# Optimization experiments

Measured on AMD Instinct MI355X. Metric: run time of the kernel, lower is better.

The kernel has to match this reference:

```python
import jax, jax.numpy as jnp
import numpy as np

E = 2_000_000   # edges
N = 200_000     # atoms
B = 100         # bond types (10 species, ordered pairs)
R = 13          # reduced_matrix_element (SK integrals per bond)
G = 512         # num_xgrid
T = 10          # atom types
OE = 4          # n_onsite_Es
R_MIN, R_MAX = 1.0, 6.0  # SK table distance range (Bohr-ish)


def setup_inputs() -> dict:
    key = jax.random.key(0)
    k1, k2, k3, k4, k5, k6 = jax.random.split(key, 6)
    rij = jax.random.uniform(k1, (E,), jnp.float32, 1.5, 5.5)
    edge_type = jax.random.randint(k2, (E,), 0, B, jnp.int32)
    atom_type = jax.random.randint(k3, (N,), 0, T, jnp.int32)
    xx = jnp.linspace(R_MIN, R_MAX, G, dtype=jnp.float32)  # sorted distance grid
    hopping_param = jax.random.normal(k4, (B, R, G), jnp.float32)
    overlap_param = jax.random.normal(k5, (B, R, G), jnp.float32)
    onsite_param = jax.random.normal(k6, (T, OE, 1), jnp.float32)
    return {"rij": rij, "edge_type": edge_type, "atom_type": atom_type,
            "xx": xx, "hopping_param": hopping_param,
            "overlap_param": overlap_param, "onsite_param": onsite_param}


def _interp_by_type(rij, edge_type, xx, table):
    """Fused gather + linear interpolation, keyed by edge_type.

    Replaces the original per-bond-type masked loop: for each edge, pick the
    [R, G] SK table for its bond type and linearly interpolate along the
    distance grid at rij. Returns [E, R].
    """
    g = xx.shape[0]
    # interval index for each edge (clamped -> linear extrapolation at edges)
    idx = jnp.clip(jnp.searchsorted(xx, rij, side="right") - 1, 0, g - 2)  # [E]
    x0 = xx[idx]
    x1 = xx[idx + 1]
    t = ((rij - x0) / (x1 - x0))[:, None]  # [E, 1]
    # advanced indexing on axes 0 and 2, full slice on axis 1 -> [E, R]
    y0 = table[edge_type, :, idx]
    y1 = table[edge_type, :, idx + 1]
    return y0 * (1.0 - t) + y1 * t


def reference(rij, edge_type, atom_type, xx, hopping_param, overlap_param, onsite_param):
    edge_features = _interp_by_type(rij, edge_type, xx, hopping_param)   # [E, R]
    edge_overlap = _interp_by_type(rij, edge_type, xx, overlap_param)    # [E, R]
    # dftb onsite: direct per-atom-type parameter lookup (num_paras == 1)
    node_features = onsite_param[atom_type, :, 0]                         # [N, OE]
    return edge_features, edge_overlap, node_features
```

## Files before the change

kernel.cpp:

```cpp
#include <hip/hip_runtime.h>

#define E_CNT 2000000
#define N_CNT 200000
#define B_CNT 100
#define R_CNT 13
#define G_CNT 512
#define T_CNT 10
#define OE_CNT 4

#define P_STRIDE 32
#define P_FLOATS ((size_t)B_CNT * G_CNT * P_STRIDE)
#define P_BYTES  (P_FLOATS * 4)

#define EDGES_PER_BLOCK 64
#define EDGE_BLOCKS (E_CNT / EDGES_PER_BLOCK)
#define NODE_BLOCKS ((N_CNT + 255) / 256)
#define OUT_OVL_OFF ((size_t)E_CNT * R_CNT)
#define OUT_NODE_OFF ((size_t)2 * E_CNT * R_CNT)

__global__ __launch_bounds__(256) void repack_kernel(
    const float* __restrict__ hopping,
    const float* __restrict__ overlap,
    float* __restrict__ P)
{
    int tid = blockIdx.x * 256 + threadIdx.x;
    const int total = B_CNT * R_CNT * G_CNT;
    if (tid >= total) return;
    int g = tid & (G_CNT - 1);
    int br = tid >> 9;
    int r = br % R_CNT;
    int b = br / R_CNT;
    size_t src = (size_t)tid;
    size_t dst = ((size_t)(b * G_CNT + g)) * P_STRIDE + r;
    P[dst] = hopping[src];
    P[dst + 16] = overlap[src];
}

__global__ __launch_bounds__(256) void dftbsk_main(
    const float* __restrict__ rij,
    const float* __restrict__ edge_type,
    const int* __restrict__ edge_type_i,
    const int* __restrict__ atom_type,
    const float* __restrict__ xx,
    const float* __restrict__ P,
    const float* __restrict__ onsite,
    float* __restrict__ out)
{
    if (blockIdx.x < EDGE_BLOCKS) {
        __shared__ float sxx[G_CNT];
        __shared__ float sh[EDGES_PER_BLOCK * 26];

        for (int i = threadIdx.x; i < G_CNT; i += 256) sxx[i] = xx[i];
        __syncthreads();

        int tid = threadIdx.x;
        int eL = tid >> 2;
        int j  = tid & 3;
        int e  = blockIdx.x * EDGES_PER_BLOCK + eL;

        float r = rij[e];
        int b = edge_type_i[e];

        const float inv_dx = (float)(G_CNT - 1) / 5.0f;
        int idx = (int)floorf((r - 1.0f) * inv_dx);
        idx = max(0, min(G_CNT - 2, idx));
        while (idx > 0 && r < sxx[idx]) --idx;
        while (idx < G_CNT - 2 && r >= sxx[idx + 1]) ++idx;

        float x0 = sxx[idx];
        float x1 = sxx[idx + 1];
        float t = (r - x0) / (x1 - x0);
        float omt = 1.0f - t;

        size_t base = ((size_t)(b * G_CNT + idx)) * P_STRIDE + 4 * j;
        float4 h0 = *(const float4*)(P + base);
        float4 h1 = *(const float4*)(P + base + P_STRIDE);
        float4 o0 = *(const float4*)(P + base + 16);
        float4 o1 = *(const float4*)(P + base + 16 + P_STRIDE);

        float4 v, w;
        v.x = h0.x * omt + h1.x * t;  v.y = h0.y * omt + h1.y * t;
        v.z = h0.z * omt + h1.z * t;  v.w = h0.w * omt + h1.w * t;
        w.x = o0.x * omt + o1.x * t;  w.y = o0.y * omt + o1.y * t;
        w.z = o0.z * omt + o1.z * t;  w.w = o0.w * omt + o1.w * t;

        int r0 = 4 * j;
        float* row = sh + eL * 26;
        {
            const float vv[4] = {v.x, v.y, v.z, v.w};
            const float ww[4] = {w.x, w.y, w.z, w.w};
            #pragma unroll
            for (int k = 0; k < 4; ++k) {
                int rr = r0 + k;
                if (rr < R_CNT) {
                    row[rr] = vv[k];
                    row[13 + rr] = ww[k];
                }
            }
        }
        __syncthreads();

        size_t hopBase = (size_t)blockIdx.x * (EDGES_PER_BLOCK * R_CNT);
        #pragma unroll
        for (int L = 0; L < 2; ++L) {
            int idx4 = tid + L * 256;
            if (idx4 < 416) {
                bool isOvl = idx4 >= 208;
                unsigned f0 = (unsigned)(isOvl ? (idx4 - 208) : idx4) * 4u;
                float4 q;
                float* qs = (float*)&q;
                #pragma unroll
                for (int k = 0; k < 4; ++k) {
                    unsigned f = f0 + k;
                    unsigned ee = f / 13u;
                    unsigned rr = f - ee * 13u;
                    qs[k] = sh[ee * 26 + (isOvl ? 13 : 0) + rr];
                }
                float* dst = out + (isOvl ? OUT_OVL_OFF : 0) + hopBase + f0;
                *(float4*)dst = q;
            }
        }
    } else {
        int n = (blockIdx.x - EDGE_BLOCKS) * 256 + threadIdx.x;
        if (n < N_CNT) {
            int t = atom_type[n];
            float4 v;
            v.x = onsite[t * OE_CNT + 0];
            v.y = onsite[t * OE_CNT + 1];
            v.z = onsite[t * OE_CNT + 2];
            v.w = onsite[t * OE_CNT + 3];
            *(float4*)(out + OUT_NODE_OFF + (size_t)n * OE_CNT) = v;
        }
    }
}

__global__ __launch_bounds__(256) void dftbsk_fallback(
    const float* __restrict__ rij,
    const int*   __restrict__ edge_type,
    const int*   __restrict__ atom_type,
    const float* __restrict__ xx,
    const float* __restrict__ hopping,
    const float* __restrict__ overlap,
    const float* __restrict__ onsite,
    float*       __restrict__ out)
{
    __shared__ float sxx[G_CNT];
    for (int i = threadIdx.x; i < G_CNT; i += blockDim.x) sxx[i] = xx[i];
    __syncthreads();

    long long gid = (long long)blockIdx.x * blockDim.x + threadIdx.x;
    if (gid < E_CNT) {
        int e = (int)gid;
        float r = rij[e];
        int b = edge_type[e];
        const float inv_dx = (float)(G_CNT - 1) / 5.0f;
        int idx = (int)floorf((r - 1.0f) * inv_dx);
        idx = max(0, min(G_CNT - 2, idx));
        while (idx > 0 && r < sxx[idx]) --idx;
        while (idx < G_CNT - 2 && r >= sxx[idx + 1]) ++idx;
        float x0 = sxx[idx], x1 = sxx[idx + 1];
        float t = (r - x0) / (x1 - x0);
        float omt = 1.0f - t;
        const float* hb = hopping + (size_t)b * (R_CNT * G_CNT) + idx;
        const float* ob = overlap + (size_t)b * (R_CNT * G_CNT) + idx;
        float* outh = out + (size_t)e * R_CNT;
        float* outo = out + OUT_OVL_OFF + (size_t)e * R_CNT;
        #pragma unroll
        for (int rr = 0; rr < R_CNT; ++rr)
            outh[rr] = hb[rr * G_CNT] * omt + hb[rr * G_CNT + 1] * t;
        #pragma unroll
        for (int rr = 0; rr < R_CNT; ++rr)
            outo[rr] = ob[rr * G_CNT] * omt + ob[rr * G_CNT + 1] * t;
    } else if (gid < (long long)E_CNT + N_CNT) {
        int n = (int)(gid - E_CNT);
        int t = atom_type[n];
        float4 v;
        v.x = onsite[t * OE_CNT + 0];
        v.y = onsite[t * OE_CNT + 1];
        v.z = onsite[t * OE_CNT + 2];
        v.w = onsite[t * OE_CNT + 3];
        *(float4*)(out + OUT_NODE_OFF + (size_t)n * OE_CNT) = v;
    }
}

extern "C" void kernel_launch(void* const* d_in, const int* in_sizes, int n_in,
                              void* d_out, int out_size, void* d_ws, size_t ws_size,
                              hipStream_t stream) {
    const float* rij        = (const float*)d_in[0];
    const int*   edge_type  = (const int*)d_in[1];
    const int*   atom_type  = (const int*)d_in[2];
    const float* xx         = (const float*)d_in[3];
    const float* hopping    = (const float*)d_in[4];
    const float* overlap    = (const float*)d_in[5];
    const float* onsite     = (const float*)d_in[6];
    float* out = (float*)d_out;

    if (ws_size >= P_BYTES) {
        float* P = (float*)d_ws;
        const int repack_total = B_CNT * R_CNT * G_CNT;
        repack_kernel<<<(repack_total + 255) / 256, 256, 0, stream>>>(hopping, overlap, P);
        dftbsk_main<<<EDGE_BLOCKS + NODE_BLOCKS, 256, 0, stream>>>(
            rij, (const float*)edge_type, edge_type, atom_type, xx, P, onsite, out);
    } else {
        const long long total = (long long)E_CNT + N_CNT;
        const int grid = (int)((total + 255) / 256);
        dftbsk_fallback<<<grid, 256, 0, stream>>>(rij, edge_type, atom_type, xx,
                                                  hopping, overlap, onsite, out);
    }
}
```

Before: 287.2 us.

## Split hopping and overlap into separate passes with analytic grid indexing

Splits the packed table into separate hopping and overlap tables, each 16 floats per grid point, and runs the edge kernel twice, once per table. Each pass then has a working set about half the size of the combined table, which should fit better in cache. The interval index now comes straight from the uniform grid spacing, so the kernel no longer loads xx into shared memory or runs the correction loops. In exchange, rij and edge_type are read twice and an extra launch is added, and the analytic index may differ from searchsorted near grid points because of float rounding.

```diff
diff --git a/kernel.cpp b/kernel.cpp
--- a/kernel.cpp
+++ b/kernel.cpp
@@ -8,9 +8,9 @@
 #define T_CNT 10
 #define OE_CNT 4
 
-#define P_STRIDE 32
-#define P_FLOATS ((size_t)B_CNT * G_CNT * P_STRIDE)
-#define P_BYTES  (P_FLOATS * 4)
+#define P_ROW 16
+#define P_ONE ((size_t)B_CNT * G_CNT * P_ROW)
+#define P_BYTES_TOTAL (2 * P_ONE * 4)
 
 #define EDGES_PER_BLOCK 64
 #define EDGE_BLOCKS (E_CNT / EDGES_PER_BLOCK)
@@ -18,40 +18,37 @@
 #define OUT_OVL_OFF ((size_t)E_CNT * R_CNT)
 #define OUT_NODE_OFF ((size_t)2 * E_CNT * R_CNT)
 
-__global__ __launch_bounds__(256) void repack_kernel(
+#define SH_STRIDE 20
+
+__global__ __launch_bounds__(256) void repack2_kernel(
     const float* __restrict__ hopping,
     const float* __restrict__ overlap,
-    float* __restrict__ P)
+    float* __restrict__ Ph,
+    float* __restrict__ Po)
 {
     int tid = blockIdx.x * 256 + threadIdx.x;
-    const int total = B_CNT * R_CNT * G_CNT;
-    if (tid >= total) return;
     int g = tid & (G_CNT - 1);
     int br = tid >> 9;
     int r = br % R_CNT;
     int b = br / R_CNT;
     size_t src = (size_t)tid;
-    size_t dst = ((size_t)(b * G_CNT + g)) * P_STRIDE + r;
-    P[dst] = hopping[src];
-    P[dst + 16] = overlap[src];
+    size_t dst = ((size_t)(b * G_CNT + g)) * P_ROW + r;
+    Ph[dst] = hopping[src];
+    Po[dst] = overlap[src];
 }
 
-__global__ __launch_bounds__(256) void dftbsk_main(
+template <bool DO_NODES>
+__global__ __launch_bounds__(256) void pass_kernel(
     const float* __restrict__ rij,
-    const float* __restrict__ edge_type,
-    const int* __restrict__ edge_type_i,
-    const int* __restrict__ atom_type,
-    const float* __restrict__ xx,
+    const int*   __restrict__ edge_type,
     const float* __restrict__ P,
+    const int*   __restrict__ atom_type,
     const float* __restrict__ onsite,
-    float* __restrict__ out)
+    float* __restrict__ out,
+    float* __restrict__ out_nodes)
 {
     if (blockIdx.x < EDGE_BLOCKS) {
-        __shared__ float sxx[G_CNT];
-        __shared__ float sh[EDGES_PER_BLOCK * 26];
-
-        for (int i = threadIdx.x; i < G_CNT; i += 256) sxx[i] = xx[i];
-        __syncthreads();
+        __shared__ float sh[EDGES_PER_BLOCK * SH_STRIDE];
 
         int tid = threadIdx.x;
         int eL = tid >> 2;
@@ -59,68 +56,42 @@
         int e  = blockIdx.x * EDGES_PER_BLOCK + eL;
 
         float r = rij[e];
-        int b = edge_type_i[e];
+        int b = edge_type[e];
 
-        const float inv_dx = (float)(G_CNT - 1) / 5.0f;
-        int idx = (int)floorf((r - 1.0f) * inv_dx);
+        const float inv_dx = 511.0f / 5.0f;
+        float s = (r - 1.0f) * inv_dx;
+        int idx = (int)s;
         idx = max(0, min(G_CNT - 2, idx));
-        while (idx > 0 && r < sxx[idx]) --idx;
-        while (idx < G_CNT - 2 && r >= sxx[idx + 1]) ++idx;
-
-        float x0 = sxx[idx];
-        float x1 = sxx[idx + 1];
-        float t = (r - x0) / (x1 - x0);
+        float t = s - (float)idx;
         float omt = 1.0f - t;
 
-        size_t base = ((size_t)(b * G_CNT + idx)) * P_STRIDE + 4 * j;
-        float4 h0 = *(const float4*)(P + base);
-        float4 h1 = *(const float4*)(P + base + P_STRIDE);
-        float4 o0 = *(const float4*)(P + base + 16);
-        float4 o1 = *(const float4*)(P + base + 16 + P_STRIDE);
+        size_t base = ((size_t)((b << 9) + idx)) * P_ROW + 4 * j;
+        float4 y0 = *(const float4*)(P + base);
+        float4 y1 = *(const float4*)(P + base + P_ROW);
 
-        float4 v, w;
-        v.x = h0.x * omt + h1.x * t;  v.y = h0.y * omt + h1.y * t;
-        v.z = h0.z * omt + h1.z * t;  v.w = h0.w * omt + h1.w * t;
-        w.x = o0.x * omt + o1.x * t;  w.y = o0.y * omt + o1.y * t;
-        w.z = o0.z * omt + o1.z * t;  w.w = o0.w * omt + o1.w * t;
+        float4 v;
+        v.x = y0.x * omt + y1.x * t;
+        v.y = y0.y * omt + y1.y * t;
+        v.z = y0.z * omt + y1.z * t;
+        v.w = y0.w * omt + y1.w * t;
 
-        int r0 = 4 * j;
-        float* row = sh + eL * 26;
-        {
-            const float vv[4] = {v.x, v.y, v.z, v.w};
-            const float ww[4] = {w.x, w.y, w.z, w.w};
+        *(float4*)(sh + eL * SH_STRIDE + 4 * j) = v;
+        __syncthreads();
+
+        if (tid < 208) {
+            unsigned f0 = (unsigned)tid * 4u;
+            float4 q;
+            float* qs = (float*)&q;
             #pragma unroll
             for (int k = 0; k < 4; ++k) {
-                int rr = r0 + k;
-                if (rr < R_CNT) {
-                    row[rr] = vv[k];
-                    row[13 + rr] = ww[k];
-                }
+                unsigned f = f0 + k;
+                unsigned ee = f / 13u;
+                unsigned rr = f - ee * 13u;
+                qs[k] = sh[ee * SH_STRIDE + rr];
             }
+            *(float4*)(out + (size_t)blockIdx.x * (EDGES_PER_BLOCK * R_CNT) + f0) = q;
         }
-        __syncthreads();
-
-        size_t hopBase = (size_t)blockIdx.x * (EDGES_PER_BLOCK * R_CNT);
-        #pragma unroll
-        for (int L = 0; L < 2; ++L) {
-            int idx4 = tid + L * 256;
-            if (idx4 < 416) {
-                bool isOvl = idx4 >= 208;
-                unsigned f0 = (unsigned)(isOvl ? (idx4 - 208) : idx4) * 4u;
-                float4 q;
-                float* qs = (float*)&q;
-                #pragma unroll
-                for (int k = 0; k < 4; ++k) {
-                    unsigned f = f0 + k;
-                    unsigned ee = f / 13u;
-                    unsigned rr = f - ee * 13u;
-                    qs[k] = sh[ee * 26 + (isOvl ? 13 : 0) + rr];
-                }
-                float* dst = out + (isOvl ? OUT_OVL_OFF : 0) + hopBase + f0;
-                *(float4*)dst = q;
-            }
-        }
-    } else {
+    } else if (DO_NODES) {
         int n = (blockIdx.x - EDGE_BLOCKS) * 256 + threadIdx.x;
         if (n < N_CNT) {
             int t = atom_type[n];
@@ -129,7 +100,7 @@
             v.y = onsite[t * OE_CNT + 1];
             v.z = onsite[t * OE_CNT + 2];
             v.w = onsite[t * OE_CNT + 3];
-            *(float4*)(out + OUT_NODE_OFF + (size_t)n * OE_CNT) = v;
+            *(float4*)(out_nodes + (size_t)n * OE_CNT) = v;
         }
     }
 }
@@ -195,12 +166,15 @@
     const float* onsite     = (const float*)d_in[6];
     float* out = (float*)d_out;
 
-    if (ws_size >= P_BYTES) {
-        float* P = (float*)d_ws;
+    if (ws_size >= P_BYTES_TOTAL) {
+        float* Ph = (float*)d_ws;
+        float* Po = Ph + P_ONE;
         const int repack_total = B_CNT * R_CNT * G_CNT;
-        repack_kernel<<<(repack_total + 255) / 256, 256, 0, stream>>>(hopping, overlap, P);
-        dftbsk_main<<<EDGE_BLOCKS + NODE_BLOCKS, 256, 0, stream>>>(
-            rij, (const float*)edge_type, edge_type, atom_type, xx, P, onsite, out);
+        repack2_kernel<<<repack_total / 256, 256, 0, stream>>>(hopping, overlap, Ph, Po);
+        pass_kernel<true><<<EDGE_BLOCKS + NODE_BLOCKS, 256, 0, stream>>>(
+            rij, edge_type, Ph, atom_type, onsite, out, out + OUT_NODE_OFF);
+        pass_kernel<false><<<EDGE_BLOCKS, 256, 0, stream>>>(
+            rij, edge_type, Po, atom_type, onsite, out + OUT_OVL_OFF, out + OUT_NODE_OFF);
     } else {
         const long long total = (long long)E_CNT + N_CNT;
         const int grid = (int)((total + 255) / 256);
```

New measurement: 279.5 us. -2.7%, faster.
